# Optimization experiments

Hardware: AMD Instinct MI355X
Metric: run time of the kernel (lower is better)

## Reference

```python
import jax, jax.numpy as jnp
import numpy as np

H = 4  # n_heads in nn.MultiheadAttention
LN_EPS = 1e-5


def _mha_seq1(x_q, x_kv, in_w, in_b, out_w, out_b):
    """torch nn.MultiheadAttention with batch_first and seq_len=1 on q and kv.
    x_q, x_kv: [B, F]. in_w: [3F, F] (packed q/k/v), out_w: [F, F].
    With a single kv position, softmax over the kv axis is identically 1,
    so the output equals out_proj(v); we still compute scores/softmax so the
    math (and zero grads to Wq/Wk) matches torch exactly.
    """
    B, F = x_q.shape
    dh = F // H
    wq, wk, wv = jnp.split(in_w, 3, axis=0)
    bq, bk, bv = jnp.split(in_b, 3, axis=0)
    q = (x_q @ wq.T + bq).reshape(B, H, dh)
    k = (x_kv @ wk.T + bk).reshape(B, H, dh)
    v = (x_kv @ wv.T + bv).reshape(B, H, dh)
    s = jnp.einsum('bhd,bhd->bh', q, k) / jnp.sqrt(jnp.asarray(dh, x_q.dtype))
    w = jax.nn.softmax(s[..., None], axis=-1)  # [B, H, 1] == 1
    o = (w * v).reshape(B, F)
    return o @ out_w.T + out_b


def _layer_norm(x, g, b):
    mu = jnp.mean(x, axis=-1, keepdims=True)
    var = jnp.mean(jnp.square(x - mu), axis=-1, keepdims=True)
    return (x - mu) * jax.lax.rsqrt(var + LN_EPS) * g + b


def setup_inputs() -> dict:
    key = jax.random.key(0)
    B, GD, TD, F = 16384, 1024, 1024, 2048
    ks = jax.random.split(key, 20)
    s = 0.02  # weight init scale
    return {
        'graph_feat': jax.random.normal(ks[0], (B, GD), jnp.float32),
        'temporal_feat': jax.random.normal(ks[1], (B, TD), jnp.float32),
        'gp_w': jax.random.normal(ks[2], (F, GD), jnp.float32) * s,
        'gp_b': jax.random.normal(ks[3], (F,), jnp.float32) * s,
        'tp_w': jax.random.normal(ks[4], (F, TD), jnp.float32) * s,
        'tp_b': jax.random.normal(ks[5], (F,), jnp.float32) * s,
        'in1_w': jax.random.normal(ks[6], (3 * F, F), jnp.float32) * s,
        'in1_b': jax.random.normal(ks[7], (3 * F,), jnp.float32) * s,
        'out1_w': jax.random.normal(ks[8], (F, F), jnp.float32) * s,
        'out1_b': jax.random.normal(ks[9], (F,), jnp.float32) * s,
        'in2_w': jax.random.normal(ks[10], (3 * F, F), jnp.float32) * s,
        'in2_b': jax.random.normal(ks[11], (3 * F,), jnp.float32) * s,
        'out2_w': jax.random.normal(ks[12], (F, F), jnp.float32) * s,
        'out2_b': jax.random.normal(ks[13], (F,), jnp.float32) * s,
        'gate_w': jax.random.normal(ks[14], (F, 2 * F), jnp.float32) * s,
        'gate_b': jax.random.normal(ks[15], (F,), jnp.float32) * s,
        'ln_g': jnp.ones((F,), jnp.float32),
        'ln_b': jnp.zeros((F,), jnp.float32),
        'lin_w': jax.random.normal(ks[16], (F, F), jnp.float32) * s,
        'lin_b': jax.random.normal(ks[17], (F,), jnp.float32) * s,
    }


def reference(graph_feat, temporal_feat, gp_w, gp_b, tp_w, tp_b,
              in1_w, in1_b, out1_w, out1_b, in2_w, in2_b, out2_w, out2_b,
              gate_w, gate_b, ln_g, ln_b, lin_w, lin_b):
    g = graph_feat @ gp_w.T + gp_b          # [B, F]
    t = temporal_feat @ tp_w.T + tp_b       # [B, F]
    attn1 = _mha_seq1(g, t, in1_w, in1_b, out1_w, out1_b)  # cross1(g, t, t)
    attn2 = _mha_seq1(t, g, in2_w, in2_b, out2_w, out2_b)  # cross2(t, g, g)
    cross = attn1 + attn2
    gate = jax.nn.sigmoid(jnp.concatenate([g, cross], axis=-1) @ gate_w.T + gate_b)
    fused = gate * g + (1.0 - gate) * cross
    fused = _layer_norm(fused + g, ln_g, ln_b)
    return fused @ lin_w.T + lin_b
```

## Files before the change

kernel.cpp:

```cpp
#include <hip/hip_runtime.h>
#include <stdint.h>

typedef __attribute__((ext_vector_type(8))) short short8;
typedef __attribute__((ext_vector_type(4))) float f32x4;

__device__ __forceinline__ unsigned short f2bf(float f) {
  union { float f; uint32_t u; } v; v.f = f;
  uint32_t u = v.u;
  u += 0x7FFF + ((u >> 16) & 1);
  return (unsigned short)(u >> 16);
}
__device__ __forceinline__ float bf2f(unsigned short h) {
  union { uint32_t u; float f; } v; v.u = ((uint32_t)h) << 16;
  return v.f;
}

__global__ void conv_kernel(const float* __restrict__ in,
                            unsigned short* __restrict__ out, int n) {
  long i = ((long)blockIdx.x * blockDim.x + threadIdx.x) * 8;
  if (i >= n) return;
  float4 a = *(const float4*)(in + i);
  float4 b = *(const float4*)(in + i + 4);
  short8 s;
  s[0] = (short)f2bf(a.x); s[1] = (short)f2bf(a.y);
  s[2] = (short)f2bf(a.z); s[3] = (short)f2bf(a.w);
  s[4] = (short)f2bf(b.x); s[5] = (short)f2bf(b.y);
  s[6] = (short)f2bf(b.z); s[7] = (short)f2bf(b.w);
  *(short8*)(out + i) = s;
}

__global__ void convcat_kernel(const float* __restrict__ in,
                               unsigned short* __restrict__ out,
                               int colbase, int n) {
  long i = ((long)blockIdx.x * blockDim.x + threadIdx.x) * 8;
  if (i >= n) return;
  float4 a = *(const float4*)(in + i);
  float4 b = *(const float4*)(in + i + 4);
  short8 s;
  s[0] = (short)f2bf(a.x); s[1] = (short)f2bf(a.y);
  s[2] = (short)f2bf(a.z); s[3] = (short)f2bf(a.w);
  s[4] = (short)f2bf(b.x); s[5] = (short)f2bf(b.y);
  s[6] = (short)f2bf(b.z); s[7] = (short)f2bf(b.w);
  long row = i >> 10, col = i & 1023;
  *(short8*)(out + row * 2048 + colbase + col) = s;
}

__global__ void convs_kernel(const float* __restrict__ in,
                             const float* __restrict__ scale,
                             unsigned short* __restrict__ out, int n) {
  long i = ((long)blockIdx.x * blockDim.x + threadIdx.x) * 8;
  if (i >= n) return;
  short8 s;
#pragma unroll
  for (int j = 0; j < 8; ++j)
    s[j] = (short)f2bf(in[i + j] * scale[(i + j) & 2047]);
  *(short8*)(out + i) = s;
}

__global__ void tconv_kernel(const float* __restrict__ in, int R, int C,
                             unsigned short* __restrict__ out) {
  __shared__ float tile[32][33];
  int c0 = blockIdx.x * 32, r0 = blockIdx.y * 32;
  int tx = threadIdx.x, ty = threadIdx.y;
#pragma unroll
  for (int i = 0; i < 32; i += 8)
    tile[ty + i][tx] = in[(long)(r0 + ty + i) * C + c0 + tx];
  __syncthreads();
#pragma unroll
  for (int i = 0; i < 32; i += 8)
    out[(long)(c0 + ty + i) * R + r0 + tx] = f2bf(tile[tx][ty + i]);
}

enum { CE_PLAIN = 0, CE_WT = 1, CE_ACC = 2 };

template <int CE>
__global__ __launch_bounds__(256)
void compose_kernel(const unsigned short* __restrict__ A, int lda,
                    const unsigned short* __restrict__ W, int ldw,
                    unsigned short* C, int ldc,
                    unsigned short* Ct, long ctoff,
                    int K, int nmt,
                    int pairBase, long aoff, long woff, long coff) {
  constexpr int BK = 32;
  __shared__ unsigned short sA[128 * BK];
  __shared__ unsigned short sB[128 * BK];
  const int tid  = threadIdx.x;
  const int lane = tid & 63;
  const int wave = tid >> 6;
  const int wr = (wave >> 1) * 64;
  const int wc = (wave & 1) * 64;

  int bid = blockIdx.x;
  if (bid >= pairBase) {
    bid -= pairBase;
    A += aoff; W += woff; C += coff; Ct += ctoff;
  }
  const long tileM = (long)(bid % nmt) * 128;
  const long tileN = (long)(bid / nmt) * 128;

  const unsigned short* gA = A + (tileM + (tid >> 2)) * (long)lda + (tid & 3) * 8;
  const unsigned short* gB = W + (tileN + (tid >> 2)) * (long)ldw + (tid & 3) * 8;
  unsigned short* lA = sA + wave * 512;
  unsigned short* lB = sB + wave * 512;

  f32x4 acc[4][4] = {};
  const int fr = lane & 15;
  const int kb = (lane >> 4) * 8;

  for (int k0 = 0; k0 < K; k0 += BK) {
    __builtin_amdgcn_global_load_lds(
        (const __attribute__((address_space(1))) void*)(gA + k0),
        (__attribute__((address_space(3))) void*)(lA), 16, 0, 0);
    __builtin_amdgcn_global_load_lds(
        (const __attribute__((address_space(1))) void*)(gA + k0 + 64 * (long)lda),
        (__attribute__((address_space(3))) void*)(lA + 2048), 16, 0, 0);
    __builtin_amdgcn_global_load_lds(
        (const __attribute__((address_space(1))) void*)(gB + k0),
        (__attribute__((address_space(3))) void*)(lB), 16, 0, 0);
    __builtin_amdgcn_global_load_lds(
        (const __attribute__((address_space(1))) void*)(gB + k0 + 64 * (long)ldw),
        (__attribute__((address_space(3))) void*)(lB + 2048), 16, 0, 0);
    __syncthreads();

    short8 aF[4], bF[4];
#pragma unroll
    for (int m = 0; m < 4; ++m)
      aF[m] = *(const short8*)&sA[(wr + m * 16 + fr) * BK + kb];
#pragma unroll
    for (int n = 0; n < 4; ++n)
      bF[n] = *(const short8*)&sB[(wc + n * 16 + fr) * BK + kb];
#pragma unroll
    for (int m = 0; m < 4; ++m)
#pragma unroll
      for (int n = 0; n < 4; ++n)
        acc[m][n] = __builtin_amdgcn_mfma_f32_16x16x32_bf16(aF[m], bF[n], acc[m][n], 0, 0, 0);
    __syncthreads();
  }

  const int cr = (lane >> 4) * 4;
  const int cc = lane & 15;
#pragma unroll
  for (int m = 0; m < 4; ++m) {
    long r0 = tileM + wr + m * 16 + cr;
#pragma unroll
    for (int n = 0; n < 4; ++n) {
      long c = tileN + wc + n * 16 + cc;
#pragma unroll
      for (int r = 0; r < 4; ++r) {
        long idx = (r0 + r) * (long)ldc + c;
        float v = acc[m][n][r];
        if constexpr (CE == CE_ACC) v += bf2f(C[idx]);
        unsigned short bv = f2bf(v);
        C[idx] = bv;
        if constexpr (CE == CE_WT) Ct[c * 2048 + (r0 + r)] = bv;
      }
    }
  }
}

enum { EPI_BIAS = 0, EPI_LNF32 = 4 };

#define VMW(N) asm volatile("s_waitcnt vmcnt(" #N ")" ::: "memory")
#define SBAR() __builtin_amdgcn_s_barrier()
#define SCB() __builtin_amdgcn_sched_barrier(0)

#define STG(D, OP, HALF, PTR, LD8)                                            \
  { char* lp_ = (char*)smem + ((D)*65536 + (OP)*32768 + (HALF)*16384 + w*2048); \
    __builtin_amdgcn_global_load_lds(                                         \
        (const __attribute__((address_space(1))) void*)(PTR),                 \
        (__attribute__((address_space(3))) void*)lp_, 16, 0, 0);              \
    __builtin_amdgcn_global_load_lds(                                         \
        (const __attribute__((address_space(1))) void*)((PTR) + (LD8)),       \
        (__attribute__((address_space(3))) void*)(lp_ + 1024), 16, 0, 0);     \
    (PTR) += 64; }
#define NOSTG ((void)0)

#define RDA(D, KK) ((KK) ? ((D) ? pA11 : pA01) : ((D) ? pA10 : pA00))
#define RDB(D, KK) ((KK) ? ((D) ? pB11 : pB01) : ((D) ? pB10 : pB00))

template <int EPI, int SWZ>
__global__ __launch_bounds__(512, 2)
void gemm8p_kernel(const unsigned short* __restrict__ A, int lda,
                   const unsigned short* __restrict__ W, int ldw,
                   int K, int ldc, int nmt,
                   const float* __restrict__ bias,
                   const float* __restrict__ bias2,
                   const float2* __restrict__ stats,
                   void* Cv) {
  __shared__ unsigned short smem[65536];

  const int tid = threadIdx.x, lane = tid & 63, w = tid >> 6;
  const int wm = w >> 2, wn = w & 3;

  int bid = blockIdx.x;
  int mt, nt;
  if (SWZ) {
    const int xcd = bid & 7, seq = bid >> 3;
    nt = seq >> 3;
    mt = xcd * 8 + (seq & 7);
  } else {
    mt = bid % nmt;
    nt = bid / nmt;
  }
  const long tileM = (long)mt * 256, tileN = (long)nt * 256;

  const int sRow = w * 16 + (lane >> 3);
  const int sCol = (((lane & 7) ^ ((lane >> 3) & 7)) * 8);
  const unsigned short* pSA0 = A + (tileM + sRow) * (long)lda + sCol;
  const unsigned short* pSA1 = pSA0 + 128 * (long)lda;
  const unsigned short* pSB0 = W + (tileN + sRow) * (long)ldw + sCol;
  const unsigned short* pSB1 = pSB0 + 128 * (long)ldw;
  const long lda8 = 8 * (long)lda, ldw8 = 8 * (long)ldw;

  const int fr = lane & 15, kc = lane >> 4, l7 = lane & 7;
  const char* pA00 = (const char*)smem + (wm * 16 + fr) * 128 + ((kc) ^ l7) * 16;
  const char* pA01 = (const char*)smem + (wm * 16 + fr) * 128 + ((4 + kc) ^ l7) * 16;
  const char* pA10 = pA00 + 65536;
  const char* pA11 = pA01 + 65536;
  const char* pB00 = (const char*)smem + 32768 + (wn * 16 + fr) * 128 + ((kc) ^ l7) * 16;
  const char* pB01 = (const char*)smem + 32768 + (wn * 16 + fr) * 128 + ((4 + kc) ^ l7) * 16;
  const char* pB10 = pB00 + 65536;
  const char* pB11 = pB01 + 65536;

  f32x4 acc[8][4] = {};
  short8 aH[4][2];
  short8 bqS[2][2][2];

#define PHASE(D, MQ, NQ, LA, LB, STGX)                                        \
  {                                                                           \
    if (LA) {                                                                 \
      _Pragma("unroll") for (int mi = 0; mi < 4; ++mi) {                      \
        aH[mi][0] = *(const short8*)(RDA(D, 0) + (MQ)*16384 + mi * 4096);     \
        aH[mi][1] = *(const short8*)(RDA(D, 1) + (MQ)*16384 + mi * 4096);     \
      }                                                                       \
    }                                                                         \
    if (LB) {                                                                 \
      _Pragma("unroll") for (int ni = 0; ni < 2; ++ni) {                      \
        bqS[NQ][ni][0] = *(const short8*)(RDB(D, 0) + (NQ)*16384 + ni * 8192);\
        bqS[NQ][ni][1] = *(const short8*)(RDB(D, 1) + (NQ)*16384 + ni * 8192);\
      }                                                                       \
    }                                                                         \
    STGX;                                                                     \
    SCB();                                                                    \
    __builtin_amdgcn_s_setprio(1);                                            \
    _Pragma("unroll") for (int mi = 0; mi < 4; ++mi)                          \
    _Pragma("unroll") for (int ni = 0; ni < 2; ++ni) {                        \
      acc[(MQ)*4+mi][(NQ)*2+ni] = __builtin_amdgcn_mfma_f32_16x16x32_bf16(    \
          aH[mi][0], bqS[NQ][ni][0], acc[(MQ)*4+mi][(NQ)*2+ni], 0, 0, 0);     \
      acc[(MQ)*4+mi][(NQ)*2+ni] = __builtin_amdgcn_mfma_f32_16x16x32_bf16(    \
          aH[mi][1], bqS[NQ][ni][1], acc[(MQ)*4+mi][(NQ)*2+ni], 0, 0, 0);     \
    }                                                                         \
    __builtin_amdgcn_s_setprio(0);                                            \
    SCB();                                                                    \
  }

  STG(0, 0, 0, pSA0, lda8);
  STG(0, 1, 0, pSB0, ldw8);
  STG(0, 1, 1, pSB1, ldw8);
  STG(0, 0, 1, pSA1, lda8);
  STG(1, 0, 0, pSA0, lda8);
  STG(1, 1, 0, pSB0, ldw8);
  STG(1, 1, 1, pSB1, ldw8);
  STG(1, 0, 1, pSA1, lda8);
  VMW(12);
  SBAR();

  const int NIT = K / 128;
  for (int it = 0; it < NIT - 1; ++it) {
    PHASE(0, 0, 0, 1, 1, NOSTG);                               VMW(10); SBAR();
    PHASE(0, 0, 1, 0, 1, STG(0, 0, 0, pSA0, lda8);
                         STG(0, 1, 0, pSB0, ldw8));            VMW(12); SBAR();
    PHASE(0, 1, 0, 1, 0, STG(0, 1, 1, pSB1, ldw8));                     SBAR();
    PHASE(0, 1, 1, 0, 0, STG(0, 0, 1, pSA1, lda8));            VMW(12); SBAR();
    PHASE(1, 0, 0, 1, 1, NOSTG);                               VMW(10); SBAR();
    PHASE(1, 0, 1, 0, 1, STG(1, 0, 0, pSA0, lda8);
                         STG(1, 1, 0, pSB0, ldw8));            VMW(12); SBAR();
    PHASE(1, 1, 0, 1, 0, STG(1, 1, 1, pSB1, ldw8));                     SBAR();
    PHASE(1, 1, 1, 0, 0, STG(1, 0, 1, pSA1, lda8));            VMW(12); SBAR();
  }
  {
    PHASE(0, 0, 0, 1, 1, NOSTG); VMW(10); SBAR();
    PHASE(0, 0, 1, 0, 1, NOSTG); VMW(8);  SBAR();
    PHASE(0, 1, 0, 1, 0, NOSTG);          SBAR();
    PHASE(0, 1, 1, 0, 0, NOSTG); VMW(4);  SBAR();
    PHASE(1, 0, 0, 1, 1, NOSTG); VMW(2);  SBAR();
    PHASE(1, 0, 1, 0, 1, NOSTG); VMW(0);  SBAR();
    PHASE(1, 1, 0, 1, 0, NOSTG);          SBAR();
    PHASE(1, 1, 1, 0, 0, NOSTG);
  }
#undef PHASE

  const int cr = (lane >> 4) * 4;
  const int cc = lane & 15;
#pragma unroll
  for (int m = 0; m < 8; ++m) {
    long rr = tileM + (m >> 2) * 128 + (m & 3) * 32 + wm * 16 + cr;
#pragma unroll
    for (int n = 0; n < 4; ++n) {
      long c = tileN + (n >> 1) * 128 + (n & 1) * 64 + wn * 16 + cc;
      float b1 = bias ? bias[c] : 0.0f;
      float b2 = bias2 ? bias2[c] : 0.0f;
#pragma unroll
      for (int r = 0; r < 4; ++r) {
        long row = rr + r;
        long idx = row * (long)ldc + c;
        float v = acc[m][n][r];
        if constexpr (EPI == EPI_BIAS) {
          ((unsigned short*)Cv)[idx] = f2bf(v + b1 + b2);
        }
        if constexpr (EPI == EPI_LNF32) {
          float2 st = stats[row];
          ((float*)Cv)[idx] = v * st.y - st.y * st.x * b1 + b2;
        }
      }
    }
  }
}

__global__ __launch_bounds__(256) void fusestats_kernel(
    const unsigned short* __restrict__ CL, const unsigned short* __restrict__ G,
    unsigned short* __restrict__ PL, float2* __restrict__ stats) {
  const int row = blockIdx.x;
  const int t = threadIdx.x, lane = t & 63, wave = t >> 6;
  short8 xc = *(const short8*)&CL[(long)row * 4096 + t * 8];
  short8 xl = *(const short8*)&CL[(long)row * 4096 + 2048 + t * 8];
  short8 xg = *(const short8*)&G[(long)row * 2048 + t * 8];
  short8 o8;
  float s = 0.f, s2 = 0.f;
#pragma unroll
  for (int j = 0; j < 8; ++j) {
    float cv = bf2f((unsigned short)xc[j]);
    float lv = bf2f((unsigned short)xl[j]);
    float gv = bf2f((unsigned short)xg[j]);
    float gt = 1.0f / (1.0f + expf(-lv));
    unsigned short pb = f2bf(gt * gv + (1.0f - gt) * cv + gv);
    o8[j] = (short)pb;
    float x = bf2f(pb);
    s += x; s2 += x * x;
  }
  *(short8*)(PL + (long)row * 2048 + t * 8) = o8;
#pragma unroll
  for (int off = 1; off < 64; off <<= 1) {
    s  += __shfl_xor(s, off);
    s2 += __shfl_xor(s2, off);
  }
  __shared__ float red[8];
  if (lane == 0) { red[wave] = s; red[4 + wave] = s2; }
  __syncthreads();
  if (t == 0) {
    float ts  = red[0] + red[1] + red[2] + red[3];
    float ts2 = red[4] + red[5] + red[6] + red[7];
    float mean = ts * (1.0f / 2048.0f);
    float var  = ts2 * (1.0f / 2048.0f) - mean * mean;
    stats[row] = make_float2(mean, rsqrtf(var + 1e-5f));
  }
}

__device__ __forceinline__ float blkRed(float s, float* red, int lane, int wave) {
#pragma unroll
  for (int off = 1; off < 64; off <<= 1) s += __shfl_xor(s, off);
  if (lane == 0) red[wave] = s;
  __syncthreads();
  return red[0] + red[1] + red[2] + red[3];
}

__global__ __launch_bounds__(256) void biascompP_kernel(
    const unsigned short* __restrict__ wO1b, const unsigned short* __restrict__ wO2b,
    const unsigned short* __restrict__ Wc1, const unsigned short* __restrict__ Wc2,
    const float* __restrict__ bv1, const float* __restrict__ bv2,
    const float* __restrict__ tpb, const float* __restrict__ gpb,
    const float* __restrict__ o1b, const float* __restrict__ o2b,
    float* __restrict__ bcV) {
  __shared__ float red[4];
  int c = blockIdx.x, t = threadIdx.x, lane = t & 63, wave = t >> 6;
  int k = t * 8;
  float s = 0.f;
  short8 a1 = *(const short8*)(wO1b + (long)c * 2048 + k);
  short8 a2 = *(const short8*)(wO2b + (long)c * 2048 + k);
  short8 a3 = *(const short8*)(Wc1 + (long)c * 2048 + k);
  short8 a4 = *(const short8*)(Wc2 + (long)c * 2048 + k);
#pragma unroll
  for (int j = 0; j < 8; ++j)
    s += bf2f((unsigned short)a1[j]) * bv1[k + j]
       + bf2f((unsigned short)a2[j]) * bv2[k + j]
       + bf2f((unsigned short)a3[j]) * tpb[k + j]
       + bf2f((unsigned short)a4[j]) * gpb[k + j];
  float tot = blkRed(s, red, lane, wave);
  if (t == 0) bcV[c] = tot + o1b[c] + o2b[c];
}

__global__ __launch_bounds__(256) void bgateP_kernel(
    const float* __restrict__ gate_w, const float* __restrict__ gate_b,
    const float* __restrict__ gpb, const float* __restrict__ bcV,
    float* __restrict__ bgateV) {
  __shared__ float red[4];
  int n = blockIdx.x, t = threadIdx.x, lane = t & 63, wave = t >> 6;
  const float* row = gate_w + (long)n * 4096;
  float s = 0.f;
  int k = t * 8;
#pragma unroll
  for (int j = 0; j < 8; ++j)
    s += row[k + j] * gpb[k + j] + row[2048 + k + j] * bcV[k + j];
  float tot = blkRed(s, red, lane, wave);
  if (t == 0) bgateV[n] = tot + gate_b[n];
}

__global__ __launch_bounds__(256) void uvP_kernel(
    const unsigned short* __restrict__ wlinp, const float* __restrict__ lin_w,
    const float* __restrict__ ln_beta, const float* __restrict__ lin_b,
    float* __restrict__ uV, float* __restrict__ vV) {
  __shared__ float redu[4], redv[4];
  int n = blockIdx.x, t = threadIdx.x, lane = t & 63, wave = t >> 6;
  int k = t * 8;
  short8 a1 = *(const short8*)(wlinp + (long)n * 2048 + k);
  float u = 0.f, v = 0.f;
#pragma unroll
  for (int j = 0; j < 8; ++j) {
    u += bf2f((unsigned short)a1[j]);
    v += ln_beta[k + j] * lin_w[(long)n * 2048 + k + j];
  }
#pragma unroll
  for (int off = 1; off < 64; off <<= 1) {
    u += __shfl_xor(u, off);
    v += __shfl_xor(v, off);
  }
  if (lane == 0) { redu[wave] = u; redv[wave] = v; }
  __syncthreads();
  if (t == 0) {
    uV[n] = redu[0] + redu[1] + redu[2] + redu[3];
    vV[n] = redv[0] + redv[1] + redv[2] + redv[3] + lin_b[n];
  }
}

extern "C" void kernel_launch(void* const* d_in, const int* in_sizes, int n_in,
                              void* d_out, int out_size, void* d_ws, size_t ws_size,
                              hipStream_t stream) {
  const float* graph    = (const float*)d_in[0];
  const float* temporal = (const float*)d_in[1];
  const float* gp_w  = (const float*)d_in[2];
  const float* gp_b  = (const float*)d_in[3];
  const float* tp_w  = (const float*)d_in[4];
  const float* tp_b  = (const float*)d_in[5];
  const float* in1_w = (const float*)d_in[6];
  const float* in1_b = (const float*)d_in[7];
  const float* out1_w = (const float*)d_in[8];
  const float* out1_b = (const float*)d_in[9];
  const float* in2_w = (const float*)d_in[10];
  const float* in2_b = (const float*)d_in[11];
  const float* out2_w = (const float*)d_in[12];
  const float* out2_b = (const float*)d_in[13];
  const float* gate_w = (const float*)d_in[14];
  const float* gate_b = (const float*)d_in[15];
  const float* ln_g  = (const float*)d_in[16];
  const float* ln_b  = (const float*)d_in[17];
  const float* lin_w = (const float*)d_in[18];
  const float* lin_b = (const float*)d_in[19];

  const int Bm = 16384, F = 2048, GD = 1024;
  const long BF = (long)Bm * F, FF = (long)F * F, FG = (long)F * GD;

  unsigned short* TG   = (unsigned short*)d_ws;
  unsigned short* PL   = TG;
  unsigned short* Gbuf = TG + BF;
  unsigned short* wLIN = Gbuf + BF;
  unsigned short* wGP  = wLIN + FF;
  unsigned short* Wcg  = wGP + FG;
  unsigned short* Wcross = Wcg;
  unsigned short* Wgate  = Wcg + FF;
  float* bc2V   = (float*)(Wcg + 2 * FF);
  float* uV     = bc2V + 2 * F;
  float* vV     = uV + F;
  float2* stats = (float2*)(vV + F);

  unsigned short* DO      = (unsigned short*)d_out;
  unsigned short* wv1T    = DO;
  unsigned short* wv2T    = wv1T + FF;
  unsigned short* tpT     = wv2T + FF;
  unsigned short* gpT     = tpT + FG;
  unsigned short* Wc1     = gpT + FG;
  unsigned short* Wc2     = Wc1 + FF;
  unsigned short* wO1b    = Wc2 + FF;
  unsigned short* wO2b    = wO1b + FF;
  unsigned short* wGATEb  = wO2b + FF;
  unsigned short* WcrossT = wGATEb + 2 * FF;
  unsigned short* CL      = DO;

  auto conv = [&](const float* src, unsigned short* dst, long n) {
    conv_kernel<<<dim3((unsigned)(n / 8 / 256)), 256, 0, stream>>>(src, dst, (int)n);
  };
  convcat_kernel<<<dim3((unsigned)(Bm * GD / 8 / 256)), 256, 0, stream>>>(
      temporal, TG, 0, Bm * GD);
  convcat_kernel<<<dim3((unsigned)(Bm * GD / 8 / 256)), 256, 0, stream>>>(
      graph, TG, GD, Bm * GD);
  conv(gp_w, wGP, FG);
  conv(out1_w, wO1b, FF);
  conv(out2_w, wO2b, FF);
  conv(gate_w, wGATEb, 2 * FF);
  convs_kernel<<<dim3((unsigned)(FF / 8 / 256)), 256, 0, stream>>>(lin_w, ln_g, wLIN, (int)FF);
  tconv_kernel<<<dim3(F / 32, F / 32), dim3(32, 8), 0, stream>>>(in1_w + 2 * FF, F, F, wv1T);
  tconv_kernel<<<dim3(F / 32, F / 32), dim3(32, 8), 0, stream>>>(in2_w + 2 * FF, F, F, wv2T);
  tconv_kernel<<<dim3(GD / 32, F / 32), dim3(32, 8), 0, stream>>>(tp_w, F, GD, tpT);
  tconv_kernel<<<dim3(GD / 32, F / 32), dim3(32, 8), 0, stream>>>(gp_w, F, GD, gpT);

  compose_kernel<CE_PLAIN><<<dim3(512), dim3(256), 0, stream>>>(
      wO1b, F, wv1T, F, Wc1, F, nullptr, 0, F, 16,
      256, wO2b - wO1b, wv2T - wv1T, Wc2 - Wc1);
  compose_kernel<CE_WT><<<dim3(256), dim3(256), 0, stream>>>(
      Wc1, F, tpT, F, Wcross, F, WcrossT, (long)1024 * 2048, F, 16,
      128, Wc2 - Wc1, gpT - tpT, 1024);
  biascompP_kernel<<<dim3(F), dim3(256), 0, stream>>>(
      wO1b, wO2b, Wc1, Wc2, in1_b + 2 * F, in2_b + 2 * F, tp_b, gp_b,
      out1_b, out2_b, bc2V);
  compose_kernel<CE_PLAIN><<<dim3(256), dim3(256), 0, stream>>>(
      wGATEb + F, 2 * F, WcrossT, F, Wgate, F, nullptr, 0, F, 16,
      1 << 30, 0, 0, 0);
  compose_kernel<CE_ACC><<<dim3(128), dim3(256), 0, stream>>>(
      wGATEb, 2 * F, gpT, F, Wgate + GD, F, nullptr, 0, F, 16,
      1 << 30, 0, 0, 0);
  bgateP_kernel<<<dim3(F), dim3(256), 0, stream>>>(gate_w, gate_b, gp_b, bc2V,
                                                   bc2V + F);
  uvP_kernel<<<dim3(F), dim3(256), 0, stream>>>(wLIN, lin_w, ln_b, lin_b, uV, vV);

  dim3 blk(512);
  gemm8p_kernel<EPI_BIAS, 1><<<dim3(512), blk, 0, stream>>>(
      TG + GD, F, wGP, GD, GD, F, 0,
      gp_b, nullptr, nullptr, Gbuf);
  gemm8p_kernel<EPI_BIAS, 1><<<dim3(1024), blk, 0, stream>>>(
      TG, F, Wcg, F, F, 2 * F, 0,
      bc2V, nullptr, nullptr, CL);
  fusestats_kernel<<<dim3(Bm), dim3(256), 0, stream>>>(CL, Gbuf, PL, stats);
  gemm8p_kernel<EPI_LNF32, 1><<<dim3(512), blk, 0, stream>>>(
      PL, F, wLIN, F, F, F, 0,
      uV, vV, stats, (void*)d_out);
}
```

Measured before the change: 806.9 us.

## Restructure GEMM main loop into four wider phases with rescheduled global prefetch

Each K-step of the bf16 MFMA GEMM inner loop now runs in four phases instead of eight. Each phase loads one A half-tile together with both B quarters and issues 32 MFMAs, where before it issued 16. Global-to-LDS staging is redistributed so the A1 tile of stage 1 is issued later and the other loads are grouped. The scheduling barrier before the MFMA block is dropped so LDS reads can interleave with the math. The aim is fewer barriers and waitcnts per K-step and better overlap of loads with MFMA, at the cost of more live B registers and possibly tighter timing on LDS buffer reuse.

```diff
diff --git a/kernel.cpp b/kernel.cpp
--- a/kernel.cpp
+++ b/kernel.cpp
@@ -226,29 +226,31 @@
   short8 aH[4][2];
   short8 bqS[2][2][2];
 
-#define PHASE(D, MQ, NQ, LA, LB, STGX)                                        \
+#define MPHASE(D, MQ, LB, STGX)                                               \
   {                                                                           \
-    if (LA) {                                                                 \
-      _Pragma("unroll") for (int mi = 0; mi < 4; ++mi) {                      \
-        aH[mi][0] = *(const short8*)(RDA(D, 0) + (MQ)*16384 + mi * 4096);     \
-        aH[mi][1] = *(const short8*)(RDA(D, 1) + (MQ)*16384 + mi * 4096);     \
+    _Pragma("unroll") for (int mi = 0; mi < 2; ++mi) {                        \
+      aH[mi][0] = *(const short8*)(RDA(D, 0) + (MQ)*16384 + mi * 4096);       \
+      aH[mi][1] = *(const short8*)(RDA(D, 1) + (MQ)*16384 + mi * 4096);       \
+    }                                                                         \
+    if (LB) {                                                                 \
+      _Pragma("unroll") for (int q = 0; q < 2; ++q)                           \
+      _Pragma("unroll") for (int ni = 0; ni < 2; ++ni) {                      \
+        bqS[q][ni][0] = *(const short8*)(RDB(D, 0) + q * 16384 + ni * 8192);  \
+        bqS[q][ni][1] = *(const short8*)(RDB(D, 1) + q * 16384 + ni * 8192);  \
       }                                                                       \
     }                                                                         \
-    if (LB) {                                                                 \
-      _Pragma("unroll") for (int ni = 0; ni < 2; ++ni) {                      \
-        bqS[NQ][ni][0] = *(const short8*)(RDB(D, 0) + (NQ)*16384 + ni * 8192);\
-        bqS[NQ][ni][1] = *(const short8*)(RDB(D, 1) + (NQ)*16384 + ni * 8192);\
-      }                                                                       \
+    _Pragma("unroll") for (int mi = 2; mi < 4; ++mi) {                        \
+      aH[mi][0] = *(const short8*)(RDA(D, 0) + (MQ)*16384 + mi * 4096);       \
+      aH[mi][1] = *(const short8*)(RDA(D, 1) + (MQ)*16384 + mi * 4096);       \
     }                                                                         \
     STGX;                                                                     \
-    SCB();                                                                    \
     __builtin_amdgcn_s_setprio(1);                                            \
     _Pragma("unroll") for (int mi = 0; mi < 4; ++mi)                          \
-    _Pragma("unroll") for (int ni = 0; ni < 2; ++ni) {                        \
-      acc[(MQ)*4+mi][(NQ)*2+ni] = __builtin_amdgcn_mfma_f32_16x16x32_bf16(    \
-          aH[mi][0], bqS[NQ][ni][0], acc[(MQ)*4+mi][(NQ)*2+ni], 0, 0, 0);     \
-      acc[(MQ)*4+mi][(NQ)*2+ni] = __builtin_amdgcn_mfma_f32_16x16x32_bf16(    \
-          aH[mi][1], bqS[NQ][ni][1], acc[(MQ)*4+mi][(NQ)*2+ni], 0, 0, 0);     \
+    _Pragma("unroll") for (int n = 0; n < 4; ++n) {                           \
+      acc[(MQ)*4+mi][n] = __builtin_amdgcn_mfma_f32_16x16x32_bf16(            \
+          aH[mi][0], bqS[n >> 1][n & 1][0], acc[(MQ)*4+mi][n], 0, 0, 0);      \
+      acc[(MQ)*4+mi][n] = __builtin_amdgcn_mfma_f32_16x16x32_bf16(            \
+          aH[mi][1], bqS[n >> 1][n & 1][1], acc[(MQ)*4+mi][n], 0, 0, 0);      \
     }                                                                         \
     __builtin_amdgcn_s_setprio(0);                                            \
     SCB();                                                                    \
@@ -261,34 +263,27 @@
   STG(1, 0, 0, pSA0, lda8);
   STG(1, 1, 0, pSB0, ldw8);
   STG(1, 1, 1, pSB1, ldw8);
-  STG(1, 0, 1, pSA1, lda8);
-  VMW(12);
+  VMW(8);
   SBAR();
 
   const int NIT = K / 128;
   for (int it = 0; it < NIT - 1; ++it) {
-    PHASE(0, 0, 0, 1, 1, NOSTG);                               VMW(10); SBAR();
-    PHASE(0, 0, 1, 0, 1, STG(0, 0, 0, pSA0, lda8);
-                         STG(0, 1, 0, pSB0, ldw8));            VMW(12); SBAR();
-    PHASE(0, 1, 0, 1, 0, STG(0, 1, 1, pSB1, ldw8));                     SBAR();
-    PHASE(0, 1, 1, 0, 0, STG(0, 0, 1, pSA1, lda8));            VMW(12); SBAR();
-    PHASE(1, 0, 0, 1, 1, NOSTG);                               VMW(10); SBAR();
-    PHASE(1, 0, 1, 0, 1, STG(1, 0, 0, pSA0, lda8);
-                         STG(1, 1, 0, pSB0, ldw8));            VMW(12); SBAR();
-    PHASE(1, 1, 0, 1, 0, STG(1, 1, 1, pSB1, ldw8));                     SBAR();
-    PHASE(1, 1, 1, 0, 0, STG(1, 0, 1, pSA1, lda8));            VMW(12); SBAR();
+    MPHASE(0, 0, 1, STG(1, 0, 1, pSA1, lda8));            VMW(8); SBAR();
+    MPHASE(0, 1, 0, STG(0, 0, 0, pSA0, lda8);
+                    STG(0, 1, 0, pSB0, ldw8);
+                    STG(0, 1, 1, pSB1, ldw8));            VMW(8); SBAR();
+    MPHASE(1, 0, 1, STG(0, 0, 1, pSA1, lda8));            VMW(8); SBAR();
+    MPHASE(1, 1, 0, STG(1, 0, 0, pSA0, lda8);
+                    STG(1, 1, 0, pSB0, ldw8);
+                    STG(1, 1, 1, pSB1, ldw8));            VMW(8); SBAR();
   }
   {
-    PHASE(0, 0, 0, 1, 1, NOSTG); VMW(10); SBAR();
-    PHASE(0, 0, 1, 0, 1, NOSTG); VMW(8);  SBAR();
-    PHASE(0, 1, 0, 1, 0, NOSTG);          SBAR();
-    PHASE(0, 1, 1, 0, 0, NOSTG); VMW(4);  SBAR();
-    PHASE(1, 0, 0, 1, 1, NOSTG); VMW(2);  SBAR();
-    PHASE(1, 0, 1, 0, 1, NOSTG); VMW(0);  SBAR();
-    PHASE(1, 1, 0, 1, 0, NOSTG);          SBAR();
-    PHASE(1, 1, 1, 0, 0, NOSTG);
-  }
-#undef PHASE
+    MPHASE(0, 0, 1, STG(1, 0, 1, pSA1, lda8)); VMW(8); SBAR();
+    MPHASE(0, 1, 0, NOSTG);                    VMW(2); SBAR();
+    MPHASE(1, 0, 1, NOSTG);                    VMW(0); SBAR();
+    MPHASE(1, 1, 0, NOSTG);
+  }
+#undef MPHASE
 
   const int cr = (lane >> 4) * 4;
   const int cc = lane & 15;
```

Measured after the change: 818.5 us. No clear change (+1.4%).
